# Performance work log

Measured on AMD Instinct MI355X. Metric: run time of the kernel, lower is better.

The kernel has to match this reference:

```python
import jax, jax.numpy as jnp
import numpy as np

B, S, D, H, F = 4, 2048, 1024, 16, 4096
DH = D // H
EPS = 1e-6


def setup_inputs() -> dict:
    key = jax.random.key(0)
    ks = jax.random.split(key, 8)
    sc = 1.0 / np.sqrt(D)
    return {
        "x": jax.random.normal(ks[0], (B, S, D), jnp.float32),
        "wq": jax.random.normal(ks[1], (D, D), jnp.float32) * sc,
        "bq": jnp.zeros((D,), jnp.float32),
        "wk": jax.random.normal(ks[2], (D, D), jnp.float32) * sc,
        "bk": jnp.zeros((D,), jnp.float32),
        "wv": jax.random.normal(ks[3], (D, D), jnp.float32) * sc,
        "bv": jnp.zeros((D,), jnp.float32),
        "wo": jax.random.normal(ks[4], (D, D), jnp.float32) * sc,
        "bo": jnp.zeros((D,), jnp.float32),
        "w1": jax.random.normal(ks[5], (D, F), jnp.float32) * sc,
        "b1": jnp.zeros((F,), jnp.float32),
        "w2": jax.random.normal(ks[6], (F, D), jnp.float32) * (1.0 / np.sqrt(F)),
        "b2": jnp.zeros((D,), jnp.float32),
        "g1": jnp.ones((D,), jnp.float32),
        "be1": jnp.zeros((D,), jnp.float32),
        "g2": jnp.ones((D,), jnp.float32),
        "be2": jnp.zeros((D,), jnp.float32),
    }


def _layernorm(x, g, b):
    mu = jnp.mean(x, axis=-1, keepdims=True)
    var = jnp.mean(jnp.square(x - mu), axis=-1, keepdims=True)
    return (x - mu) * jax.lax.rsqrt(var + EPS) * g + b


def reference(x, wq, bq, wk, bk, wv, bv, wo, bo, w1, b1, w2, b2, g1, be1, g2, be2):
    # self-attention: q=k=v=x
    q = (x @ wq + bq).reshape(B, S, H, DH).transpose(0, 2, 1, 3)  # [B,H,S,DH]
    k = (x @ wk + bk).reshape(B, S, H, DH).transpose(0, 2, 1, 3)
    v = (x @ wv + bv).reshape(B, S, H, DH).transpose(0, 2, 1, 3)
    logits = jnp.einsum("bhqd,bhkd->bhqk", q, k) / jnp.sqrt(jnp.float32(DH))
    attn = jax.nn.softmax(logits, axis=-1)
    ctx = jnp.einsum("bhqk,bhkd->bhqd", attn, v)  # [B,H,S,DH]
    ctx = ctx.transpose(0, 2, 1, 3).reshape(B, S, D)
    attn_out = ctx @ wo + bo
    out1 = _layernorm(x + attn_out, g1, be1)
    ffn = jax.nn.relu(out1 @ w1 + b1) @ w2 + b2
    out2 = _layernorm(out1 + ffn, g2, be2)
    return out2
```

## Files before the change

### kernel.cpp

```cpp
#include <hip/hip_runtime.h>

typedef unsigned short u16;
typedef unsigned int u32;

typedef __attribute__((ext_vector_type(8))) short short8;
typedef __attribute__((ext_vector_type(4))) float floatx4;
typedef __attribute__((ext_vector_type(16))) float floatx16;
typedef __attribute__((ext_vector_type(2))) unsigned int uint2v;
typedef __attribute__((ext_vector_type(4))) unsigned int uint4v;

static __device__ __forceinline__ u16 f2b(float f) {
    union { float f; u32 i; } v; v.f = f;
    u32 r = v.i + 0x7fffu + ((v.i >> 16) & 1u);
    return (u16)(r >> 16);
}
static __device__ __forceinline__ float exp2f_hw(float x) {
    return __builtin_amdgcn_exp2f(x);
}
static __device__ __forceinline__ u32 cvtpk(float lo, float hi) {
    u32 r;
    asm("v_cvt_pk_bf16_f32 %0, %1, %2" : "=v"(r) : "v"(lo), "v"(hi));
    return r;
}

static __device__ __forceinline__ floatx4 mfma16(short8 a, short8 b, floatx4 c) {
    return __builtin_amdgcn_mfma_f32_16x16x32_bf16(a, b, c, 0, 0, 0);
}
static __device__ __forceinline__ floatx16 mfma32(short8 a, short8 b, floatx16 c) {
    return __builtin_amdgcn_mfma_f32_32x32x16_bf16(a, b, c, 0, 0, 0);
}

typedef __attribute__((address_space(1))) const void gas_void;
typedef __attribute__((address_space(3))) void las_void;
static __device__ __forceinline__ void gl_lds16(const void* g, void* l) {
    __builtin_amdgcn_global_load_lds((gas_void*)g, (las_void*)l, 16, 0, 0);
}

#define B_ 4
#define S_ 2048
#define D_ 1024
#define H_ 16
#define DH_ 64
#define F_ 4096
#define QKVS 3072

#define QSCALE 0.18033688011112042f

__global__ __launch_bounds__(256) void cast_b(const float* __restrict__ in,
                                              u16* __restrict__ out, int n4) {
    int id = blockIdx.x * 256 + threadIdx.x;
    if (id < n4) {
        float4 v = ((const float4*)in)[id];
        ushort4 u;
        u.x = f2b(v.x); u.y = f2b(v.y); u.z = f2b(v.z); u.w = f2b(v.w);
        ((ushort4*)out)[id] = u;
    }
}

__global__ __launch_bounds__(256) void concat_bias(const float* __restrict__ bq,
                                                   const float* __restrict__ bk,
                                                   const float* __restrict__ bv,
                                                   float* __restrict__ o) {
    int i = blockIdx.x * 256 + threadIdx.x;
    float v;
    if (i < 1024) v = bq[i] * QSCALE;
    else if (i < 2048) v = bk[i - 1024];
    else v = bv[i - 2048];
    o[i] = v;
}

__global__ void transpose_cast(const float* __restrict__ in, u16* __restrict__ out,
                               int R, int C, float scale) {
    __shared__ float t[32][33];
    int bx = blockIdx.x;
    int by = blockIdx.y;
    int x = threadIdx.x, y = threadIdx.y;
#pragma unroll
    for (int i = 0; i < 4; ++i) {
        int r = by * 32 + y + i * 8;
        t[y + i * 8][x] = in[(size_t)r * C + bx * 32 + x];
    }
    __syncthreads();
#pragma unroll
    for (int i = 0; i < 4; ++i) {
        int c = bx * 32 + y + i * 8;
        out[(size_t)c * R + by * 32 + x] = f2b(t[x][y + i * 8] * scale);
    }
}

__global__ void transpose_v(const u16* __restrict__ qkv, u16* __restrict__ vt) {
    __shared__ u16 t[32][33];
    int bh = blockIdx.z; int b = bh >> 4, h = bh & 15;
    int s0 = blockIdx.x * 32, d0 = blockIdx.y * 32;
    int x = threadIdx.x, y = threadIdx.y;
#pragma unroll
    for (int i = 0; i < 4; ++i)
        t[y + i * 8][x] =
            qkv[(size_t)(b * S_ + s0 + y + i * 8) * QKVS + 2048 + h * DH_ + d0 + x];
    __syncthreads();
#pragma unroll
    for (int i = 0; i < 4; ++i)
        vt[((size_t)bh * DH_ + d0 + y + i * 8) * S_ + s0 + x] = t[x][y + i * 8];
}

__global__ __launch_bounds__(256) void gemm_bt(const u16* __restrict__ A,
                                               const u16* __restrict__ Bt,
                                               const float* __restrict__ bias,
                                               float* __restrict__ outF,
                                               u16* __restrict__ outB,
                                               int M, int N, int K, int relu) {
    __shared__ __align__(16) u16 sA[128 * 64];
    __shared__ __align__(16) u16 sB[128 * 64];

    int tid = threadIdx.x;
    int w = tid >> 6, lane = tid & 63, quad = lane >> 4, l = lane & 15;
    int wr = w >> 1, wc = w & 1;
    int bM = blockIdx.y, bN = blockIdx.x;

    floatx4 acc[4][4];
#pragma unroll
    for (int i = 0; i < 4; ++i)
#pragma unroll
        for (int j = 0; j < 4; ++j) acc[i][j] = (floatx4){0.f, 0.f, 0.f, 0.f};

    int r = lane >> 3;
    int c = lane & 7;
    int cg = ((c ^ r) << 3);
    const u16* gA = &A[(size_t)(bM * 128 + r) * K + cg];
    const u16* gB = &Bt[(size_t)(bN * 128 + r) * K + cg];

    int l7 = l & 7;

    for (int kk = 0; kk < K; kk += 64) {
#pragma unroll
        for (int hh = 0; hh < 4; ++hh) {
            int rowbase = hh * 32 + w * 8;
            gl_lds16(gA + (size_t)rowbase * K + kk, &sA[rowbase * 64]);
            gl_lds16(gB + (size_t)rowbase * K + kk, &sB[rowbase * 64]);
        }
        __syncthreads();

#pragma unroll
        for (int kf = 0; kf < 2; ++kf) {
            int ch = ((kf * 4 + quad) ^ l7) << 3;
            short8 af[4], bfr[4];
#pragma unroll
            for (int mt = 0; mt < 4; ++mt) {
                int m = wr * 64 + mt * 16 + l;
                af[mt] = *(const short8*)&sA[m * 64 + ch];
            }
#pragma unroll
            for (int nt = 0; nt < 4; ++nt) {
                int n = wc * 64 + nt * 16 + l;
                bfr[nt] = *(const short8*)&sB[n * 64 + ch];
            }
#pragma unroll
            for (int mt = 0; mt < 4; ++mt)
#pragma unroll
                for (int nt = 0; nt < 4; ++nt)
                    acc[mt][nt] = mfma16(af[mt], bfr[nt], acc[mt][nt]);
        }
        __syncthreads();
    }

#pragma unroll
    for (int nt = 0; nt < 4; ++nt) {
        int colg = bN * 128 + wc * 64 + nt * 16 + l;
        float bv = bias ? bias[colg] : 0.f;
#pragma unroll
        for (int mt = 0; mt < 4; ++mt) {
#pragma unroll
            for (int rr = 0; rr < 4; ++rr) {
                int rowg = bM * 128 + wr * 64 + mt * 16 + quad * 4 + rr;
                float v = acc[mt][nt][rr] + bv;
                if (relu) v = fmaxf(v, 0.f);
                size_t idx = (size_t)rowg * N + colg;
                if (outF) outF[idx] = v;
                if (outB) outB[idx] = f2b(v);
            }
        }
    }
}

#define PACK8(sv, rb, dst) {                                                   \
    u32 pa_ = cvtpk(sv[rb + 0], sv[rb + 1]), pb_ = cvtpk(sv[rb + 4], sv[rb + 5]); \
    u32 pc_ = cvtpk(sv[rb + 2], sv[rb + 3]), pd_ = cvtpk(sv[rb + 6], sv[rb + 7]); \
    uint2v t0_ = __builtin_amdgcn_permlane32_swap(pa_, pb_, 0, 0);             \
    uint2v t1_ = __builtin_amdgcn_permlane32_swap(pc_, pd_, 0, 0);             \
    union { uint4v u; short8 s8; } cv_;                                        \
    cv_.u = (uint4v){t0_[0], t1_[0], t0_[1], t1_[1]};                          \
    dst = cv_.s8; }

__global__ __launch_bounds__(256, 4) void attn_kernel(const u16* __restrict__ qkv,
                                                      const u16* __restrict__ vt,
                                                      u16* __restrict__ ctx) {
    __shared__ __align__(16) u16 Kb[2][64 * 64];
    __shared__ __align__(16) u16 Vb[2][64 * 64];

    int bh = blockIdx.x; int b = bh >> 4, h = bh & 15;
    int tid = threadIdx.x;
    int w = tid >> 6, lane = tid & 63;
    int l32 = lane & 31, hi = lane >> 5, row7 = lane & 7;
    int qw = blockIdx.y * 128 + w * 32;

    int r = lane >> 3, c = lane & 7;
    int cs = ((c ^ r) << 3);
    const u16* gK0 = qkv + (size_t)(b * S_ + w * 16 + r) * QKVS + 1024 + h * DH_ + cs;
    const u16* gK1 = gK0 + (size_t)8 * QKVS;
    const u16* gV0 = vt + (size_t)(bh * DH_ + w * 16 + r) * S_ + cs;
    const u16* gV1 = gV0 + (size_t)8 * S_;

    auto stage = [&](int bb) {
        u16* lk = &Kb[bb][w * 16 * 64];
        u16* lv = &Vb[bb][w * 16 * 64];
        gl_lds16(gK0, lk);
        gl_lds16(gK1, lk + 8 * 64);
        gl_lds16(gV0, lv);
        gl_lds16(gV1, lv + 8 * 64);
        gK0 += (size_t)64 * QKVS; gK1 += (size_t)64 * QKVS;
        gV0 += 64; gV1 += 64;
    };

    short8 qf0, qf1, qf2, qf3;
    {
        const u16* qp = qkv + (size_t)(b * S_ + qw + l32) * QKVS + h * DH_ + hi * 8;
        qf0 = *(const short8*)(qp);
        qf1 = *(const short8*)(qp + 16);
        qf2 = *(const short8*)(qp + 32);
        qf3 = *(const short8*)(qp + 48);
    }

    floatx16 O0, O1;
#pragma unroll
    for (int i = 0; i < 16; ++i) { O0[i] = 0.f; O1[i] = 0.f; }
    float lra = 0.f, lrb = 0.f, lrc = 0.f, lrd = 0.f;

    int roff0 = l32 * 64;
    int roff1 = (32 + l32) * 64;

    stage(0);
    __syncthreads();

    const int NT = S_ / 64;
    for (int kt = 0; kt < NT; ++kt) {
        int cur = kt & 1;
        if (kt + 1 < NT) stage(cur ^ 1);

        const u16* Kc = Kb[cur];
        const u16* Vc = Vb[cur];

        floatx16 s0;
#pragma unroll
        for (int i = 0; i < 16; ++i) s0[i] = 0.f;
#pragma unroll
        for (int kc = 0; kc < 4; ++kc) {
            int ch = (((kc * 2 + hi) ^ row7) << 3);
            short8 ka = *(const short8*)&Kc[roff0 + ch];
            short8 qk = (kc == 0) ? qf0 : (kc == 1) ? qf1 : (kc == 2) ? qf2 : qf3;
            s0 = mfma32(ka, qk, s0);
        }
#pragma unroll
        for (int i = 0; i < 16; ++i) s0[i] = exp2f_hw(s0[i]);
        short8 pa0, pa1;
        PACK8(s0, 0, pa0);
        PACK8(s0, 8, pa1);

        floatx16 s1;
#pragma unroll
        for (int i = 0; i < 16; ++i) s1[i] = 0.f;
#pragma unroll
        for (int kc = 0; kc < 4; ++kc) {
            int ch = (((kc * 2 + hi) ^ row7) << 3);
            short8 ka = *(const short8*)&Kc[roff1 + ch];
            short8 qk = (kc == 0) ? qf0 : (kc == 1) ? qf1 : (kc == 2) ? qf2 : qf3;
            s1 = mfma32(ka, qk, s1);
        }
#pragma unroll
        for (int i = 0; i < 16; ++i) s1[i] = exp2f_hw(s1[i]);
        short8 pa2, pa3;
        PACK8(s1, 0, pa2);
        PACK8(s1, 8, pa3);

#pragma unroll
        for (int i = 0; i < 16; i += 4) {
            lra += s0[i + 0] + s1[i + 0];
            lrb += s0[i + 1] + s1[i + 1];
            lrc += s0[i + 2] + s1[i + 2];
            lrd += s0[i + 3] + s1[i + 3];
        }

        {
            short8 vb0 = *(const short8*)&Vc[roff0 + (((0 + hi) ^ row7) << 3)];
            O0 = mfma32(pa0, vb0, O0);
            short8 vb1 = *(const short8*)&Vc[roff0 + (((2 + hi) ^ row7) << 3)];
            O0 = mfma32(pa1, vb1, O0);
            short8 vb2 = *(const short8*)&Vc[roff0 + (((4 + hi) ^ row7) << 3)];
            O0 = mfma32(pa2, vb2, O0);
            short8 vb3 = *(const short8*)&Vc[roff0 + (((6 + hi) ^ row7) << 3)];
            O0 = mfma32(pa3, vb3, O0);
        }
        {
            short8 vb0 = *(const short8*)&Vc[roff1 + (((0 + hi) ^ row7) << 3)];
            O1 = mfma32(pa0, vb0, O1);
            short8 vb1 = *(const short8*)&Vc[roff1 + (((2 + hi) ^ row7) << 3)];
            O1 = mfma32(pa1, vb1, O1);
            short8 vb2 = *(const short8*)&Vc[roff1 + (((4 + hi) ^ row7) << 3)];
            O1 = mfma32(pa2, vb2, O1);
            short8 vb3 = *(const short8*)&Vc[roff1 + (((6 + hi) ^ row7) << 3)];
            O1 = mfma32(pa3, vb3, O1);
        }

        __syncthreads();
    }

    float lr = (lra + lrb) + (lrc + lrd);
    lr += __shfl_xor(lr, 32);
    float inv = 1.0f / lr;
#pragma unroll
    for (int rr = 0; rr < 16; ++rr) {
        int rowq = (rr & 3) + 8 * (rr >> 2) + 4 * hi;
        float iv = __shfl(inv, rowq);
        size_t base = (size_t)(b * S_ + qw + rowq) * D_ + h * DH_ + l32;
        ctx[base]      = f2b(O0[rr] * iv);
        ctx[base + 32] = f2b(O1[rr] * iv);
    }
}

__global__ __launch_bounds__(256) void add_ln(const float* __restrict__ a,
                                              const float* __restrict__ b,
                                              const float* __restrict__ g,
                                              const float* __restrict__ be,
                                              float* __restrict__ outF,
                                              u16* __restrict__ outB) {
    int row = blockIdx.x, tid = threadIdx.x;
    size_t base = (size_t)row * D_;
    float4 va = ((const float4*)(a + base))[tid];
    float4 vb = ((const float4*)(b + base))[tid];
    float x0 = va.x + vb.x, x1 = va.y + vb.y, x2 = va.z + vb.z, x3 = va.w + vb.w;
    float s1 = x0 + x1 + x2 + x3;
    float s2 = x0 * x0 + x1 * x1 + x2 * x2 + x3 * x3;
#pragma unroll
    for (int off = 32; off; off >>= 1) {
        s1 += __shfl_xor(s1, off);
        s2 += __shfl_xor(s2, off);
    }
    __shared__ float r1[4], r2[4];
    int w = tid >> 6, lane = tid & 63;
    if (lane == 0) { r1[w] = s1; r2[w] = s2; }
    __syncthreads();
    s1 = r1[0] + r1[1] + r1[2] + r1[3];
    s2 = r2[0] + r2[1] + r2[2] + r2[3];
    float mean = s1 * (1.0f / D_);
    float var = s2 * (1.0f / D_) - mean * mean;
    float inv = rsqrtf(var + 1e-6f);
    float4 vg = ((const float4*)g)[tid];
    float4 vbe = ((const float4*)be)[tid];
    float o0 = (x0 - mean) * inv * vg.x + vbe.x;
    float o1 = (x1 - mean) * inv * vg.y + vbe.y;
    float o2 = (x2 - mean) * inv * vg.z + vbe.z;
    float o3 = (x3 - mean) * inv * vg.w + vbe.w;
    float4 o; o.x = o0; o.y = o1; o.z = o2; o.w = o3;
    ((float4*)(outF + base))[tid] = o;
    if (outB) {
        ushort4 u;
        u.x = f2b(o0); u.y = f2b(o1); u.z = f2b(o2); u.w = f2b(o3);
        ((ushort4*)(outB + base))[tid] = u;
    }
}

extern "C" void kernel_launch(void* const* d_in, const int* in_sizes, int n_in,
                              void* d_out, int out_size, void* d_ws, size_t ws_size,
                              hipStream_t stream) {
    const float* x   = (const float*)d_in[0];
    const float* wq  = (const float*)d_in[1];
    const float* bq  = (const float*)d_in[2];
    const float* wk  = (const float*)d_in[3];
    const float* bk  = (const float*)d_in[4];
    const float* wv  = (const float*)d_in[5];
    const float* bv  = (const float*)d_in[6];
    const float* wo  = (const float*)d_in[7];
    const float* bo  = (const float*)d_in[8];
    const float* w1  = (const float*)d_in[9];
    const float* b1  = (const float*)d_in[10];
    const float* w2  = (const float*)d_in[11];
    const float* b2  = (const float*)d_in[12];
    const float* g1  = (const float*)d_in[13];
    const float* be1 = (const float*)d_in[14];
    const float* g2  = (const float*)d_in[15];
    const float* be2 = (const float*)d_in[16];
    float* out = (float*)d_out;
    char* ws = (char*)d_ws;
    const size_t MB = 1u << 20;

    u16* xb      = (u16*)(ws + 0);
    u16* wqkvT   = (u16*)(ws + 16 * MB);
    u16* woT     = (u16*)(ws + 22 * MB);
    u16* w1T     = (u16*)(ws + 24 * MB);
    u16* w2T     = (u16*)(ws + 32 * MB);
    float* qkvb  = (float*)(ws + 40 * MB);
    u16* qkv     = (u16*)(ws + 41 * MB);
    u16* vtb     = (u16*)(ws + 89 * MB);
    u16* ctxb    = (u16*)(ws + 105 * MB);
    float* attn_out = (float*)(ws + 121 * MB);
    float* out1     = (float*)(ws + 153 * MB);
    u16* out1b   = (u16*)(ws + 0);
    u16* hidden  = (u16*)(ws + 41 * MB);
    float* ffn2out = (float*)(ws + 121 * MB);

    dim3 tb(32, 8);

    cast_b<<<8192, 256, 0, stream>>>(x, xb, (B_ * S_ * D_) / 4);
    transpose_cast<<<dim3(32, 32), tb, 0, stream>>>(wq, wqkvT, D_, D_, QSCALE);
    transpose_cast<<<dim3(32, 32), tb, 0, stream>>>(wk, wqkvT + 1024 * 1024, D_, D_, 1.0f);
    transpose_cast<<<dim3(32, 32), tb, 0, stream>>>(wv, wqkvT + 2048 * 1024, D_, D_, 1.0f);
    transpose_cast<<<dim3(32, 32), tb, 0, stream>>>(wo, woT, D_, D_, 1.0f);
    transpose_cast<<<dim3(128, 32), tb, 0, stream>>>(w1, w1T, D_, F_, 1.0f);
    transpose_cast<<<dim3(32, 128), tb, 0, stream>>>(w2, w2T, F_, D_, 1.0f);
    concat_bias<<<12, 256, 0, stream>>>(bq, bk, bv, qkvb);

    gemm_bt<<<dim3(24, 64), 256, 0, stream>>>(xb, wqkvT, qkvb, nullptr, qkv,
                                              B_ * S_, QKVS, D_, 0);
    transpose_v<<<dim3(S_ / 32, DH_ / 32, B_ * H_), tb, 0, stream>>>(qkv, vtb);

    attn_kernel<<<dim3(B_ * H_, S_ / 128), 256, 0, stream>>>(qkv, vtb, ctxb);

    gemm_bt<<<dim3(8, 64), 256, 0, stream>>>(ctxb, woT, bo, attn_out, nullptr,
                                             B_ * S_, D_, D_, 0);
    add_ln<<<B_ * S_, 256, 0, stream>>>(x, attn_out, g1, be1, out1, out1b);

    gemm_bt<<<dim3(32, 64), 256, 0, stream>>>(out1b, w1T, b1, nullptr, hidden,
                                              B_ * S_, F_, D_, 1);
    gemm_bt<<<dim3(8, 64), 256, 0, stream>>>(hidden, w2T, b2, ffn2out, nullptr,
                                             B_ * S_, D_, F_, 0);
    add_ln<<<B_ * S_, 256, 0, stream>>>(out1, ffn2out, g2, be2, out, nullptr);
}
```

Baseline: 552.3 us.

## Add 256x256 pipelined GEMM kernel for QKV and FFN1 projections

Adds a new 512-thread GEMM with 256x256 output tiles. It uses a multi-stage global-to-LDS pipeline with explicit vmcnt waits and raw barriers, MFMA priority boosting, swizzled LDS layout and workgroup-order swizzling. The QKV and FFN1 GEMMs use it instead of the 128x128 kernel, to raise data reuse per tile and hide load latency. The cost is higher register and LDS use (128KB shared) and fewer workgroups, 384 and 512 tiles on 256 CUs, which can leave part of the GPU idle in the last wave.

New measurement: 551.3 us. Within noise of the previous version (-0.2%).

```diff
diff --git a/kernel.cpp b/kernel.cpp
--- a/kernel.cpp
+++ b/kernel.cpp
@@ -35,6 +35,15 @@
 static __device__ __forceinline__ void gl_lds16(const void* g, void* l) {
     __builtin_amdgcn_global_load_lds((gas_void*)g, (las_void*)l, 16, 0, 0);
 }
+
+template<int N> static __device__ __forceinline__ void vmw() {
+    if constexpr (N == 0)  asm volatile("s_waitcnt vmcnt(0)" ::: "memory");
+    else if constexpr (N == 4)  asm volatile("s_waitcnt vmcnt(4)" ::: "memory");
+    else if constexpr (N == 8)  asm volatile("s_waitcnt vmcnt(8)" ::: "memory");
+    else if constexpr (N == 9)  asm volatile("s_waitcnt vmcnt(9)" ::: "memory");
+    else if constexpr (N == 12) asm volatile("s_waitcnt vmcnt(12)" ::: "memory");
+}
+#define SBAR() asm volatile("s_barrier" ::: "memory")
 
 #define B_ 4
 #define S_ 2048
@@ -172,6 +181,134 @@
 #pragma unroll
             for (int rr = 0; rr < 4; ++rr) {
                 int rowg = bM * 128 + wr * 64 + mt * 16 + quad * 4 + rr;
+                float v = acc[mt][nt][rr] + bv;
+                if (relu) v = fmaxf(v, 0.f);
+                size_t idx = (size_t)rowg * N + colg;
+                if (outF) outF[idx] = v;
+                if (outB) outB[idx] = f2b(v);
+            }
+        }
+    }
+}
+
+#define MFMA16X(MH)                                                        \
+    __builtin_amdgcn_s_setprio(1);                                         \
+    acc[(MH)*4+0][0] = mfma16(af0, bf0, acc[(MH)*4+0][0]);                 \
+    acc[(MH)*4+0][1] = mfma16(af0, bf1, acc[(MH)*4+0][1]);                 \
+    acc[(MH)*4+0][2] = mfma16(af0, bf2, acc[(MH)*4+0][2]);                 \
+    acc[(MH)*4+0][3] = mfma16(af0, bf3, acc[(MH)*4+0][3]);                 \
+    acc[(MH)*4+1][0] = mfma16(af1, bf0, acc[(MH)*4+1][0]);                 \
+    acc[(MH)*4+1][1] = mfma16(af1, bf1, acc[(MH)*4+1][1]);                 \
+    acc[(MH)*4+1][2] = mfma16(af1, bf2, acc[(MH)*4+1][2]);                 \
+    acc[(MH)*4+1][3] = mfma16(af1, bf3, acc[(MH)*4+1][3]);                 \
+    acc[(MH)*4+2][0] = mfma16(af2, bf0, acc[(MH)*4+2][0]);                 \
+    acc[(MH)*4+2][1] = mfma16(af2, bf1, acc[(MH)*4+2][1]);                 \
+    acc[(MH)*4+2][2] = mfma16(af2, bf2, acc[(MH)*4+2][2]);                 \
+    acc[(MH)*4+2][3] = mfma16(af2, bf3, acc[(MH)*4+2][3]);                 \
+    acc[(MH)*4+3][0] = mfma16(af3, bf0, acc[(MH)*4+3][0]);                 \
+    acc[(MH)*4+3][1] = mfma16(af3, bf1, acc[(MH)*4+3][1]);                 \
+    acc[(MH)*4+3][2] = mfma16(af3, bf2, acc[(MH)*4+3][2]);                 \
+    acc[(MH)*4+3][3] = mfma16(af3, bf3, acc[(MH)*4+3][3]);                 \
+    __builtin_amdgcn_s_setprio(0);
+
+#define PPAIR(P, KH, ST0, VM0, ST1, VM1) {                                 \
+    const u16* bBp = &smem[32768 + ((P)*2 + (KH)) * 8192];                 \
+    short8 bf0 = *(const short8*)&bBp[boff];                               \
+    short8 bf1 = *(const short8*)&bBp[boff + 512];                         \
+    short8 bf2 = *(const short8*)&bBp[boff + 1024];                        \
+    short8 bf3 = *(const short8*)&bBp[boff + 1536];                        \
+    {   const u16* bAp = &smem[((P)*4 + (KH)*2 + 0) * 4096];               \
+        short8 af0 = *(const short8*)&bAp[aoff];                           \
+        short8 af1 = *(const short8*)&bAp[aoff + 512];                     \
+        short8 af2 = *(const short8*)&bAp[aoff + 1024];                    \
+        short8 af3 = *(const short8*)&bAp[aoff + 1536];                    \
+        ST0;                                                               \
+        MFMA16X(0)                                                         \
+        vmw<VM0>(); SBAR();                                                \
+    }                                                                      \
+    {   const u16* bAp = &smem[((P)*4 + (KH)*2 + 1) * 4096];               \
+        short8 af0 = *(const short8*)&bAp[aoff];                           \
+        short8 af1 = *(const short8*)&bAp[aoff + 512];                     \
+        short8 af2 = *(const short8*)&bAp[aoff + 1024];                    \
+        short8 af3 = *(const short8*)&bAp[aoff + 1536];                    \
+        ST1;                                                               \
+        MFMA16X(1)                                                         \
+        vmw<VM1>(); SBAR();                                                \
+    } }
+
+__global__ __launch_bounds__(512) void gemm256(const u16* __restrict__ A,
+                                               const u16* __restrict__ Bt,
+                                               const float* __restrict__ bias,
+                                               float* __restrict__ outF,
+                                               u16* __restrict__ outB,
+                                               int M, int N, int K, int relu) {
+    __shared__ __align__(16) u16 smem[65536];
+
+    int tid = threadIdx.x;
+    int w = tid >> 6, lane = tid & 63, quad = lane >> 4, l = lane & 15;
+    int wr = w >> 2, wc = w & 3;
+
+    int nbN = gridDim.x, nwg = gridDim.x * gridDim.y;
+    int flat = blockIdx.y * gridDim.x + blockIdx.x;
+    int swz = (flat & 7) * (nwg >> 3) + (flat >> 3);
+    int bM = swz / nbN, bN = swz % nbN;
+
+    floatx4 acc[8][4];
+#pragma unroll
+    for (int i = 0; i < 8; ++i)
+#pragma unroll
+        for (int j = 0; j < 4; ++j) acc[i][j] = (floatx4){0.f, 0.f, 0.f, 0.f};
+
+    int g8 = (((lane & 3) ^ ((lane >> 3) & 3)) << 3);
+    int rA = ((w >> 2) << 7) + ((w & 3) << 4) + (lane >> 2);
+    int rB = (w << 4) + (lane >> 2);
+    const u16* gAb = A + (size_t)(bM * 256 + rA) * K + g8;
+    const u16* gBb = Bt + (size_t)(bN * 256 + rB) * K + g8;
+
+    auto stA = [&](int p, int kh, int mh, int t) {
+        gl_lds16(gAb + (size_t)(mh * 64) * K + t * 64 + kh * 32,
+                 (void*)&smem[((p << 2) + (kh << 1) + mh) * 4096 + (w << 9)]);
+    };
+    auto stB = [&](int p, int kh, int hb, int t) {
+        gl_lds16(gBb + (size_t)(hb * 128) * K + t * 64 + kh * 32,
+                 (void*)&smem[32768 + ((p << 1) + kh) * 8192 + hb * 4096 + (w << 9)]);
+    };
+
+    int sQ = ((quad ^ ((l >> 1) & 3)) << 3);
+    int aoff = ((wr << 6) + l) * 32 + sQ;
+    int boff = ((wc << 6) + l) * 32 + sQ;
+
+    stA(0, 0, 0, 0); stA(0, 0, 1, 0); stB(0, 0, 0, 0); stB(0, 0, 1, 0);
+    stA(0, 1, 0, 0); stA(0, 1, 1, 0); stB(0, 1, 0, 0); stB(0, 1, 1, 0);
+    stA(1, 0, 0, 1); stA(1, 0, 1, 1); stB(1, 0, 0, 1); stB(1, 0, 1, 1);
+    stA(1, 1, 0, 1);
+    vmw<9>(); SBAR();
+
+    const int KT = K >> 6;
+    for (int i = 0; i < (KT >> 1) - 1; ++i) {
+        int t1 = 2 * i + 1, t2 = 2 * i + 2, t3 = 2 * i + 3;
+        PPAIR(0, 0, (stA(1,1,1,t1), stB(1,1,0,t1), stB(1,1,1,t1)), 12, (stA(0,0,0,t2)), 9)
+        PPAIR(0, 1, (stA(0,0,1,t2), stB(0,0,0,t2), stB(0,0,1,t2)), 12, (stA(0,1,0,t2)), 9)
+        PPAIR(1, 0, (stA(0,1,1,t2), stB(0,1,0,t2), stB(0,1,1,t2)), 12, (stA(1,0,0,t3)), 9)
+        PPAIR(1, 1, (stA(1,0,1,t3), stB(1,0,0,t3), stB(1,0,1,t3)), 12, (stA(1,1,0,t3)), 9)
+    }
+    {
+        int t1 = KT - 1;
+        PPAIR(0, 0, (stA(1,1,1,t1), stB(1,1,0,t1), stB(1,1,1,t1)), 12, ((void)0), 8)
+        PPAIR(0, 1, ((void)0), 8, ((void)0), 4)
+        PPAIR(1, 0, ((void)0), 4, ((void)0), 0)
+        PPAIR(1, 1, ((void)0), 0, ((void)0), 0)
+    }
+
+#pragma unroll
+    for (int nt = 0; nt < 4; ++nt) {
+        int colg = bN * 256 + wc * 64 + nt * 16 + l;
+        float bv = bias ? bias[colg] : 0.f;
+#pragma unroll
+        for (int mt = 0; mt < 8; ++mt) {
+#pragma unroll
+            for (int rr = 0; rr < 4; ++rr) {
+                int rowg = bM * 256 + wr * 128 + mt * 16 + quad * 4 + rr;
                 float v = acc[mt][nt][rr] + bv;
                 if (relu) v = fmaxf(v, 0.f);
                 size_t idx = (size_t)rowg * N + colg;
@@ -418,7 +555,7 @@
     transpose_cast<<<dim3(32, 128), tb, 0, stream>>>(w2, w2T, F_, D_, 1.0f);
     concat_bias<<<12, 256, 0, stream>>>(bq, bk, bv, qkvb);
 
-    gemm_bt<<<dim3(24, 64), 256, 0, stream>>>(xb, wqkvT, qkvb, nullptr, qkv,
+    gemm256<<<dim3(12, 32), 512, 0, stream>>>(xb, wqkvT, qkvb, nullptr, qkv,
                                               B_ * S_, QKVS, D_, 0);
     transpose_v<<<dim3(S_ / 32, DH_ / 32, B_ * H_), tb, 0, stream>>>(qkv, vtb);
 
@@ -428,7 +565,7 @@
                                              B_ * S_, D_, D_, 0);
     add_ln<<<B_ * S_, 256, 0, stream>>>(x, attn_out, g1, be1, out1, out1b);
 
-    gemm_bt<<<dim3(32, 64), 256, 0, stream>>>(out1b, w1T, b1, nullptr, hidden,
+    gemm256<<<dim3(16, 32), 512, 0, stream>>>(out1b, w1T, b1, nullptr, hidden,
                                               B_ * S_, F_, D_, 1);
     gemm_bt<<<dim3(8, 64), 256, 0, stream>>>(hidden, w2T, b2, ffn2out, nullptr,
                                              B_ * S_, D_, F_, 0);
```

## Replace GEMM with 256x256 double-buffered pipelined kernel and split-K FFN2

Applied to the files above, without the earlier changes.

Replaces the 128x128 GEMM with a 512-thread 256x256-tile kernel that double-buffers LDS stages, interleaves async global-to-LDS loads with MFMA blocks under explicit vmcnt waits and barriers, raises MFMA priority, and swizzles block order for L2 locality. The FFN2 GEMM is split along K into two partials written to separate buffers, and a new three-input add+layernorm sums them. The aim is more data reuse per tile, hidden load latency, and more parallelism for the narrow N=1024 GEMMs. In exchange the kernel needs 128KB of LDS, which limits occupancy, it assumes K is a multiple of 128, and the split-K path adds an extra fp32 write and read. The output buffer is used as scratch for one partial.

Result: no change. 556.8 us (+0.8%).

```diff
diff --git a/kernel.cpp b/kernel.cpp
--- a/kernel.cpp
+++ b/kernel.cpp
@@ -35,6 +35,12 @@
 static __device__ __forceinline__ void gl_lds16(const void* g, void* l) {
     __builtin_amdgcn_global_load_lds((gas_void*)g, (las_void*)l, 16, 0, 0);
 }
+
+template<int N> static __device__ __forceinline__ void vmw() {
+    if constexpr (N == 0)      asm volatile("s_waitcnt vmcnt(0)" ::: "memory");
+    else if constexpr (N == 4) asm volatile("s_waitcnt vmcnt(4)" ::: "memory");
+}
+#define SBAR() asm volatile("s_barrier" ::: "memory")
 
 #define B_ 4
 #define S_ 2048
@@ -103,79 +109,134 @@
         vt[((size_t)bh * DH_ + d0 + y + i * 8) * S_ + s0 + x] = t[x][y + i * 8];
 }
 
-__global__ __launch_bounds__(256) void gemm_bt(const u16* __restrict__ A,
+#define MFMA16X(MH)                                                        \
+    __builtin_amdgcn_s_setprio(1);                                         \
+    acc[(MH)*4+0][0] = mfma16(af0, bf0, acc[(MH)*4+0][0]);                 \
+    acc[(MH)*4+0][1] = mfma16(af0, bf1, acc[(MH)*4+0][1]);                 \
+    acc[(MH)*4+0][2] = mfma16(af0, bf2, acc[(MH)*4+0][2]);                 \
+    acc[(MH)*4+0][3] = mfma16(af0, bf3, acc[(MH)*4+0][3]);                 \
+    acc[(MH)*4+1][0] = mfma16(af1, bf0, acc[(MH)*4+1][0]);                 \
+    acc[(MH)*4+1][1] = mfma16(af1, bf1, acc[(MH)*4+1][1]);                 \
+    acc[(MH)*4+1][2] = mfma16(af1, bf2, acc[(MH)*4+1][2]);                 \
+    acc[(MH)*4+1][3] = mfma16(af1, bf3, acc[(MH)*4+1][3]);                 \
+    acc[(MH)*4+2][0] = mfma16(af2, bf0, acc[(MH)*4+2][0]);                 \
+    acc[(MH)*4+2][1] = mfma16(af2, bf1, acc[(MH)*4+2][1]);                 \
+    acc[(MH)*4+2][2] = mfma16(af2, bf2, acc[(MH)*4+2][2]);                 \
+    acc[(MH)*4+2][3] = mfma16(af2, bf3, acc[(MH)*4+2][3]);                 \
+    acc[(MH)*4+3][0] = mfma16(af3, bf0, acc[(MH)*4+3][0]);                 \
+    acc[(MH)*4+3][1] = mfma16(af3, bf1, acc[(MH)*4+3][1]);                 \
+    acc[(MH)*4+3][2] = mfma16(af3, bf2, acc[(MH)*4+3][2]);                 \
+    acc[(MH)*4+3][3] = mfma16(af3, bf3, acc[(MH)*4+3][3]);                 \
+    __builtin_amdgcn_s_setprio(0);
+
+#define PPAIR(P, KH, ST0, W0, ST1, W1) {                                   \
+    int ro = l * 64 + ((((KH) * 4 + quad) ^ l7) << 3);                     \
+    const u16* bBp = &smem[32768 + (P) * 16384 + wc * 4096];               \
+    short8 bf0 = *(const short8*)&bBp[ro];                                 \
+    short8 bf1 = *(const short8*)&bBp[ro + 1024];                          \
+    short8 bf2 = *(const short8*)&bBp[ro + 2048];                          \
+    short8 bf3 = *(const short8*)&bBp[ro + 3072];                          \
+    {   const u16* bAp = &smem[(P) * 16384 + (wr * 2 + 0) * 4096];         \
+        short8 af0 = *(const short8*)&bAp[ro];                             \
+        short8 af1 = *(const short8*)&bAp[ro + 1024];                      \
+        short8 af2 = *(const short8*)&bAp[ro + 2048];                      \
+        short8 af3 = *(const short8*)&bAp[ro + 3072];                      \
+        ST0; W0; SBAR();                                                   \
+        MFMA16X(0)                                                         \
+        SBAR();                                                            \
+    }                                                                      \
+    {   const u16* bAp = &smem[(P) * 16384 + (wr * 2 + 1) * 4096];         \
+        short8 af0 = *(const short8*)&bAp[ro];                             \
+        short8 af1 = *(const short8*)&bAp[ro + 1024];                      \
+        short8 af2 = *(const short8*)&bAp[ro + 2048];                      \
+        short8 af3 = *(const short8*)&bAp[ro + 3072];                      \
+        ST1; W1; SBAR();                                                   \
+        MFMA16X(1)                                                         \
+        SBAR();                                                            \
+    } }
+
+__global__ __launch_bounds__(512) void gemm256(const u16* __restrict__ A,
                                                const u16* __restrict__ Bt,
                                                const float* __restrict__ bias,
                                                float* __restrict__ outF,
+                                               float* __restrict__ outF2,
                                                u16* __restrict__ outB,
-                                               int M, int N, int K, int relu) {
-    __shared__ __align__(16) u16 sA[128 * 64];
-    __shared__ __align__(16) u16 sB[128 * 64];
+                                               int M, int N, int K, int klen,
+                                               int relu) {
+    __shared__ __align__(16) u16 smem[65536];
 
     int tid = threadIdx.x;
     int w = tid >> 6, lane = tid & 63, quad = lane >> 4, l = lane & 15;
-    int wr = w >> 1, wc = w & 1;
-    int bM = blockIdx.y, bN = blockIdx.x;
-
-    floatx4 acc[4][4];
-#pragma unroll
-    for (int i = 0; i < 4; ++i)
+    int wr = w >> 2, wc = w & 3;
+    int l7 = l & 7;
+
+    int nbN = gridDim.x, nwg = gridDim.x * gridDim.y;
+    int flat = blockIdx.y * gridDim.x + blockIdx.x;
+    int swz = (flat & 7) * (nwg >> 3) + (flat >> 3);
+    int bM = swz / nbN, bN = swz % nbN;
+    int koff = blockIdx.z * klen;
+
+    floatx4 acc[8][4];
+#pragma unroll
+    for (int i = 0; i < 8; ++i)
 #pragma unroll
         for (int j = 0; j < 4; ++j) acc[i][j] = (floatx4){0.f, 0.f, 0.f, 0.f};
 
-    int r = lane >> 3;
-    int c = lane & 7;
-    int cg = ((c ^ r) << 3);
-    const u16* gA = &A[(size_t)(bM * 128 + r) * K + cg];
-    const u16* gB = &Bt[(size_t)(bN * 128 + r) * K + cg];
-
-    int l7 = l & 7;
-
-    for (int kk = 0; kk < K; kk += 64) {
-#pragma unroll
-        for (int hh = 0; hh < 4; ++hh) {
-            int rowbase = hh * 32 + w * 8;
-            gl_lds16(gA + (size_t)rowbase * K + kk, &sA[rowbase * 64]);
-            gl_lds16(gB + (size_t)rowbase * K + kk, &sB[rowbase * 64]);
-        }
-        __syncthreads();
-
-#pragma unroll
-        for (int kf = 0; kf < 2; ++kf) {
-            int ch = ((kf * 4 + quad) ^ l7) << 3;
-            short8 af[4], bfr[4];
-#pragma unroll
-            for (int mt = 0; mt < 4; ++mt) {
-                int m = wr * 64 + mt * 16 + l;
-                af[mt] = *(const short8*)&sA[m * 64 + ch];
-            }
-#pragma unroll
-            for (int nt = 0; nt < 4; ++nt) {
-                int n = wc * 64 + nt * 16 + l;
-                bfr[nt] = *(const short8*)&sB[n * 64 + ch];
-            }
-#pragma unroll
-            for (int mt = 0; mt < 4; ++mt)
-#pragma unroll
-                for (int nt = 0; nt < 4; ++nt)
-                    acc[mt][nt] = mfma16(af[mt], bfr[nt], acc[mt][nt]);
-        }
-        __syncthreads();
-    }
-
+    int rT = tid >> 3, cT = tid & 7;
+    int cg8 = ((cT ^ (rT & 7)) << 3);
+    const u16* gA0 = A + (size_t)(bM * 256 + rT) * K + koff + cg8;
+    const u16* gB0 = Bt + (size_t)(bN * 256 + rT) * K + koff + cg8;
+
+    auto stA = [&](int p, int ch, int t) {
+        gl_lds16(gA0 + (size_t)(ch * 64) * K + t * 64,
+                 (void*)&smem[p * 16384 + ch * 4096 + (w << 9)]);
+    };
+    auto stB = [&](int p, int hb, int t) {
+        gl_lds16(gB0 + (size_t)(hb * 64) * K + t * 64,
+                 (void*)&smem[32768 + p * 16384 + hb * 4096 + (w << 9)]);
+    };
+
+    stA(0, 0, 0); stA(0, 1, 0); stA(0, 2, 0); stA(0, 3, 0);
+    stB(0, 0, 0); stB(0, 1, 0); stB(0, 2, 0); stB(0, 3, 0);
+    stA(1, 0, 1); stA(1, 2, 1); stB(1, 0, 1); stB(1, 1, 1);
+    vmw<4>(); SBAR();
+
+    const int NI = klen >> 7;
+    for (int i = 0; i < NI - 1; ++i) {
+        int t1 = 2 * i + 1, t2 = 2 * i + 2, t3 = 2 * i + 3;
+        PPAIR(0, 0, (stA(1,1,t1), stA(1,3,t1), stB(1,2,t1), stB(1,3,t1)),
+                    ((void)0), ((void)0), ((void)0))
+        PPAIR(0, 1, ((void)0), ((void)0),
+                    (stA(0,0,t2), stA(0,2,t2), stB(0,0,t2), stB(0,1,t2)), vmw<4>())
+        PPAIR(1, 0, (stA(0,1,t2), stA(0,3,t2), stB(0,2,t2), stB(0,3,t2)),
+                    ((void)0), ((void)0), ((void)0))
+        PPAIR(1, 1, ((void)0), ((void)0),
+                    (stA(1,0,t3), stA(1,2,t3), stB(1,0,t3), stB(1,1,t3)), vmw<4>())
+    }
+    {
+        int t1 = 2 * (NI - 1) + 1;
+        PPAIR(0, 0, (stA(1,1,t1), stA(1,3,t1), stB(1,2,t1), stB(1,3,t1)),
+                    ((void)0), ((void)0), ((void)0))
+        PPAIR(0, 1, ((void)0), ((void)0), ((void)0), vmw<0>())
+        PPAIR(1, 0, ((void)0), ((void)0), ((void)0), ((void)0))
+        PPAIR(1, 1, ((void)0), ((void)0), ((void)0), ((void)0))
+    }
+
+    float* of = (blockIdx.z == 0) ? outF : outF2;
+    const float* bp = (blockIdx.z == 0) ? bias : nullptr;
 #pragma unroll
     for (int nt = 0; nt < 4; ++nt) {
-        int colg = bN * 128 + wc * 64 + nt * 16 + l;
-        float bv = bias ? bias[colg] : 0.f;
-#pragma unroll
-        for (int mt = 0; mt < 4; ++mt) {
+        int colg = bN * 256 + wc * 64 + nt * 16 + l;
+        float bv = bp ? bp[colg] : 0.f;
+#pragma unroll
+        for (int mt = 0; mt < 8; ++mt) {
 #pragma unroll
             for (int rr = 0; rr < 4; ++rr) {
-                int rowg = bM * 128 + wr * 64 + mt * 16 + quad * 4 + rr;
+                int rowg = bM * 256 + wr * 128 + mt * 16 + quad * 4 + rr;
                 float v = acc[mt][nt][rr] + bv;
                 if (relu) v = fmaxf(v, 0.f);
                 size_t idx = (size_t)rowg * N + colg;
-                if (outF) outF[idx] = v;
+                if (of) of[idx] = v;
                 if (outB) outB[idx] = f2b(v);
             }
         }
@@ -366,6 +427,45 @@
         u.x = f2b(o0); u.y = f2b(o1); u.z = f2b(o2); u.w = f2b(o3);
         ((ushort4*)(outB + base))[tid] = u;
     }
+}
+
+__global__ __launch_bounds__(256) void add_ln3(const float* __restrict__ a,
+                                               const float* __restrict__ b,
+                                               const float* __restrict__ c,
+                                               const float* __restrict__ g,
+                                               const float* __restrict__ be,
+                                               float* __restrict__ outF) {
+    int row = blockIdx.x, tid = threadIdx.x;
+    size_t base = (size_t)row * D_;
+    float4 va = ((const float4*)(a + base))[tid];
+    float4 vb = ((const float4*)(b + base))[tid];
+    float4 vc = ((const float4*)(c + base))[tid];
+    float x0 = va.x + vb.x + vc.x, x1 = va.y + vb.y + vc.y;
+    float x2 = va.z + vb.z + vc.z, x3 = va.w + vb.w + vc.w;
+    float s1 = x0 + x1 + x2 + x3;
+    float s2 = x0 * x0 + x1 * x1 + x2 * x2 + x3 * x3;
+#pragma unroll
+    for (int off = 32; off; off >>= 1) {
+        s1 += __shfl_xor(s1, off);
+        s2 += __shfl_xor(s2, off);
+    }
+    __shared__ float r1[4], r2[4];
+    int w = tid >> 6, lane = tid & 63;
+    if (lane == 0) { r1[w] = s1; r2[w] = s2; }
+    __syncthreads();
+    s1 = r1[0] + r1[1] + r1[2] + r1[3];
+    s2 = r2[0] + r2[1] + r2[2] + r2[3];
+    float mean = s1 * (1.0f / D_);
+    float var = s2 * (1.0f / D_) - mean * mean;
+    float inv = rsqrtf(var + 1e-6f);
+    float4 vg = ((const float4*)g)[tid];
+    float4 vbe = ((const float4*)be)[tid];
+    float4 o;
+    o.x = (x0 - mean) * inv * vg.x + vbe.x;
+    o.y = (x1 - mean) * inv * vg.y + vbe.y;
+    o.z = (x2 - mean) * inv * vg.z + vbe.z;
+    o.w = (x3 - mean) * inv * vg.w + vbe.w;
+    ((float4*)(outF + base))[tid] = o;
 }
 
 extern "C" void kernel_launch(void* const* d_in, const int* in_sizes, int n_in,
@@ -405,7 +505,7 @@
     float* out1     = (float*)(ws + 153 * MB);
     u16* out1b   = (u16*)(ws + 0);
     u16* hidden  = (u16*)(ws + 41 * MB);
-    float* ffn2out = (float*)(ws + 121 * MB);
+    float* ffn2p0 = (float*)(ws + 121 * MB);
 
     dim3 tb(32, 8);
 
@@ -418,19 +518,19 @@
     transpose_cast<<<dim3(32, 128), tb, 0, stream>>>(w2, w2T, F_, D_, 1.0f);
     concat_bias<<<12, 256, 0, stream>>>(bq, bk, bv, qkvb);
 
-    gemm_bt<<<dim3(24, 64), 256, 0, stream>>>(xb, wqkvT, qkvb, nullptr, qkv,
-                                              B_ * S_, QKVS, D_, 0);
+    gemm256<<<dim3(12, 32, 1), 512, 0, stream>>>(xb, wqkvT, qkvb, nullptr, nullptr,
+                                                 qkv, B_ * S_, QKVS, D_, D_, 0);
     transpose_v<<<dim3(S_ / 32, DH_ / 32, B_ * H_), tb, 0, stream>>>(qkv, vtb);
 
     attn_kernel<<<dim3(B_ * H_, S_ / 128), 256, 0, stream>>>(qkv, vtb, ctxb);
 
-    gemm_bt<<<dim3(8, 64), 256, 0, stream>>>(ctxb, woT, bo, attn_out, nullptr,
-                                             B_ * S_, D_, D_, 0);
+    gemm256<<<dim3(4, 32, 1), 512, 0, stream>>>(ctxb, woT, bo, attn_out, nullptr,
+                                                nullptr, B_ * S_, D_, D_, D_, 0);
     add_ln<<<B_ * S_, 256, 0, stream>>>(x, attn_out, g1, be1, out1, out1b);
 
-    gemm_bt<<<dim3(32, 64), 256, 0, stream>>>(out1b, w1T, b1, nullptr, hidden,
-                                              B_ * S_, F_, D_, 1);
-    gemm_bt<<<dim3(8, 64), 256, 0, stream>>>(hidden, w2T, b2, ffn2out, nullptr,
-                                             B_ * S_, D_, F_, 0);
-    add_ln<<<B_ * S_, 256, 0, stream>>>(out1, ffn2out, g2, be2, out, nullptr);
-}
+    gemm256<<<dim3(16, 32, 1), 512, 0, stream>>>(out1b, w1T, b1, nullptr, nullptr,
+                                                 hidden, B_ * S_, F_, D_, D_, 1);
+    gemm256<<<dim3(4, 32, 2), 512, 0, stream>>>(hidden, w2T, b2, ffn2p0, out,
+                                                nullptr, B_ * S_, D_, F_, F_ / 2, 0);
+    add_ln3<<<B_ * S_, 256, 0, stream>>>(out1, ffn2p0, out, g2, be2, out);
+}
```
